# Optimization experiments

Measured on AMD Instinct MI355X. Metric: run time of the kernel, lower is better.

## Reference

```python
import jax, jax.numpy as jnp
import numpy as np

# Hyperparameters matching init_kwargs / repo defaults
MARGIN = 0.2
ALPHA = 0.1          # opt.alpha
OT_ITER = 20         # opt.OT_iteration
BETA = 0.5           # IPOT temperature (hardcoded in repo's OT module)
SIM_TYPE = "MISA"    # opt.sim_type_dot
MAX_VIOLATION = True
EPS = 1e-12

N_IMAGE = 128
N_REG = 36
D = 1024
MAX_WORD = 60


def _matchmap_sim(M):
    # M: (n_image, n_regions, n_word)
    if SIM_TYPE == "SISA":
        return M.mean(axis=2).mean(axis=1)
    elif SIM_TYPE == "MISA":
        return M.max(axis=1).mean(axis=1)
    elif SIM_TYPE == "SIMA":
        return M.max(axis=2).mean(axis=1)
    raise ValueError


def _ipot_distance(C, n, m):
    # C: (bs, n, m) cosine-distance cost; IPOT with uniform marginals.
    bs = C.shape[0]
    # Torch code detaches T, so no gradient flows through the iteration.
    A = jnp.exp(-jax.lax.stop_gradient(C) / BETA)

    def body(_, carry):
        T, sigma = carry
        Q = A * T                                            # (bs, n, m)
        delta = 1.0 / (n * jnp.matmul(Q, sigma))             # (bs, n, 1)
        sigma = 1.0 / (m * jnp.matmul(Q.transpose(0, 2, 1), delta))  # (bs, m, 1)
        T = delta * Q * sigma.transpose(0, 2, 1)
        return (T, sigma)

    T0 = jnp.ones((bs, n, m), C.dtype)
    s0 = jnp.ones((bs, m, 1), C.dtype) / m
    T, _ = jax.lax.fori_loop(0, OT_ITER, body, (T0, s0))
    T = jax.lax.stop_gradient(T)
    # batch_trace(C^T T) == sum(C * T) per batch element
    return -jnp.sum(C * T, axis=(1, 2))                      # (bs,)


def _scores(im, s, cap_lens):
    n_reg = im.shape[1]
    imn = im / (jnp.linalg.norm(im, axis=2, keepdims=True) + EPS)
    lens = np.asarray(cap_lens)
    sims, sims_ot = [], []
    for i in range(s.shape[0]):  # ragged per-caption loop (as in original)
        n_word = int(lens[i])
        cap = s[i, :n_word, :]                               # (w, d)
        # matchmap: bmm(images, cap^T) -> (n_image, n_regions, n_word)
        M = jnp.einsum('brd,wd->brw', im, cap)
        sims.append(_matchmap_sim(M))
        capn = cap / (jnp.linalg.norm(cap, axis=1, keepdims=True) + EPS)
        # cost_matrix_batch_torch(cap^T, img^T).transpose -> (n_image, n_reg, n_word)
        C = 1.0 - jnp.einsum('brd,wd->brw', imn, capn)
        sims_ot.append(_ipot_distance(C, n_reg, n_word))
    return jnp.stack(sims, axis=1), jnp.stack(sims_ot, axis=1)  # (n_img, n_cap)


def _loss(im, s, cap_lens):
    scores, scores_ot = _scores(im, s, cap_lens)
    n = scores.shape[0]
    eye = jnp.eye(n, dtype=bool)

    def costs(sc):
        d = jnp.diag(sc)[:, None]                            # (n, 1)
        cs = jnp.clip(MARGIN + sc - d, 0.0)                  # caption-side
        ci = jnp.clip(MARGIN + sc - d.T, 0.0)                # image-side
        cs = jnp.where(eye, 0.0, cs)
        ci = jnp.where(eye, 0.0, ci)
        return cs, ci

    cost_s, cost_im = costs(scores)
    cost_s_ot, cost_im_ot = costs(scores_ot)
    cost_s = cost_s + ALPHA * cost_s_ot
    cost_im = cost_im + ALPHA * cost_im_ot
    if MAX_VIOLATION:
        cost_s = cost_s.max(axis=1)
        cost_im = cost_im.max(axis=0)
        cost_s_ot = cost_s_ot.max(axis=1)
        cost_im_ot = cost_im_ot.max(axis=0)
    return (cost_s.sum() + cost_im.sum(), cost_s_ot.sum() + cost_im_ot.sum())


def setup_inputs() -> dict:
    key = jax.random.key(0)
    k1, k2, k3 = jax.random.split(key, 3)
    im = jax.random.normal(k1, (N_IMAGE, N_REG, D), dtype=jnp.float32)
    s = jax.random.normal(k2, (N_IMAGE, MAX_WORD, D), dtype=jnp.float32)
    rng = np.random.default_rng(0)
    s_l = np.asarray(rng.integers(10, MAX_WORD + 1, size=N_IMAGE), dtype=np.int64)
    x = jax.random.normal(k3, (1,), dtype=jnp.float32)  # unused by forward math
    return {"im": im, "s": s, "s_l": s_l, "x": x}


def reference(im, s, s_l, x):
    return _loss(im, s, s_l)
```

## Files before the change

kernel.cpp:

```cpp
#include <hip/hip_runtime.h>
#include <hip/hip_bf16.h>
#include <math.h>

#define N_IMAGE 128
#define N_REG   36
#define DIM     1024
#define MAX_WORD 60
#define OT_ITERS 20
#define MARGIN_F 0.2f
#define ALPHA_F  0.1f
#define EPS_F    1e-12f

#define APAN  16384
#define AIMG  (3 * APAN)
#define BCAP  (4 * APAN)

typedef short bf16x8 __attribute__((ext_vector_type(8)));
typedef float f32x4  __attribute__((ext_vector_type(4)));
typedef float f32x2  __attribute__((ext_vector_type(2)));


__device__ __forceinline__ unsigned int pkbf2(float a, float b) {
    union { __hip_bfloat162 h2; unsigned int u; } cv;
    cv.h2 = __float22bfloat162_rn(make_float2(a, b));
    return cv.u;
}
__device__ __forceinline__ float lo16(unsigned int u) { return __int_as_float((int)(u << 16)); }
__device__ __forceinline__ float hi16(unsigned int u) { return __int_as_float((int)(u & 0xFFFF0000u)); }

#define SWZ(x, pat) __int_as_float(__builtin_amdgcn_ds_swizzle(__float_as_int(x), (pat)))
#define BPERM(a, x) __int_as_float(__builtin_amdgcn_ds_bpermute((a), __float_as_int(x)))

__device__ __forceinline__ float bfly16_sum(float x) {
    x += SWZ(x, 0x041F);
    x += SWZ(x, 0x081F);
    x += SWZ(x, 0x101F);
    x += SWZ(x, 0x201F);
    return x;
}

__device__ __forceinline__ float xq_sum(float x) {
    x += SWZ(x, 0x401F);
    const int xaddr = (((int)(threadIdx.x & 63) ^ 32) << 2);
    x += BPERM(xaddr, x);
    return x;
}
__device__ __forceinline__ float xq_max(float x) {
    x = fmaxf(x, SWZ(x, 0x401F));
    const int xaddr = (((int)(threadIdx.x & 63) ^ 32) << 2);
    x = fmaxf(x, BPERM(xaddr, x));
    return x;
}
__device__ __forceinline__ float bfly64_sum(float x) {
    return xq_sum(bfly16_sum(x));
}


__global__ __launch_bounds__(256) void pack_kernel(
    const float* __restrict__ im, const float* __restrict__ s,
    float* __restrict__ inv_im, float* __restrict__ inv_cap,
    float* __restrict__ out,
    unsigned short* __restrict__ imp, unsigned short* __restrict__ sp) {

    const int pid = blockIdx.x;
    const int tid = threadIdx.x;
    if (pid == 0 && tid == 0) { out[0] = 0.0f; out[1] = 0.0f; }

    const int w = tid >> 6, lane = tid & 63, q = lane >> 4, l15 = lane & 15;
    const bool isim = (pid < 384);
    int obj, p, nvalid;
    const float* src;
    unsigned short* dst;
    if (isim) {
        obj = pid / 3; p = pid % 3;
        src = im + (size_t)obj * 36 * DIM;
        dst = imp + (size_t)obj * AIMG + (size_t)p * APAN;
        nvalid = 36;
    } else {
        const int k = pid - 384;
        obj = k >> 2; p = k & 3;
        src = s + (size_t)obj * 60 * DIM;
        dst = sp + (size_t)obj * BCAP + (size_t)p * APAN;
        nvalid = 60;
    }
    const int row = p * 16 + l15;
    const bool valid = (row < nvalid);

    float ss = 0.0f;
    #pragma unroll
    for (int i = 0; i < 4; ++i) {
        const int c = w * 4 + i;
        #pragma unroll
        for (int h = 0; h < 2; ++h) {
            float4 v0 = make_float4(0.f, 0.f, 0.f, 0.f), v1 = v0;
            if (valid) {
                const float* rp = src + (size_t)row * DIM + c * 64 + h * 32 + q * 8;
                v0 = *(const float4*)rp;
                v1 = *(const float4*)(rp + 4);
            }
            ss += v0.x * v0.x + v0.y * v0.y + v0.z * v0.z + v0.w * v0.w
                + v1.x * v1.x + v1.y * v1.y + v1.z * v1.z + v1.w * v1.w;
            uint4 o;
            o.x = pkbf2(v0.x, v0.y); o.y = pkbf2(v0.z, v0.w);
            o.z = pkbf2(v1.x, v1.y); o.w = pkbf2(v1.z, v1.w);
            *(uint4*)(dst + (size_t)c * 1024 + h * 512 + q * 128 + l15 * 8) = o;
        }
    }
    ss = xq_sum(ss);
    __shared__ float sh[4][16];
    if (lane < 16) sh[w][lane] = ss;
    __syncthreads();
    if (tid < 16) {
        const float t = sh[0][tid] + sh[1][tid] + sh[2][tid] + sh[3][tid];
        const int r = p * 16 + tid;
        if (r < nvalid) {
            const float inv = 1.0f / (sqrtf(t) + EPS_F);
            if (isim) inv_im[obj * 36 + r] = inv;
            else      inv_cap[obj * 60 + r] = inv;
        }
    }
}


__global__ void norms_kernel(const float* __restrict__ im, const float* __restrict__ s,
                             float* __restrict__ inv_im, float* __restrict__ inv_cap,
                             float* __restrict__ out) {
    if (blockIdx.x == 0 && threadIdx.x == 0) { out[0] = 0.0f; out[1] = 0.0f; }
    const int NIM = N_IMAGE * N_REG;
    const int NS  = N_IMAGE * MAX_WORD;
    int row  = blockIdx.x * 4 + (threadIdx.x >> 6);
    int lane = threadIdx.x & 63;
    if (row >= NIM + NS) return;
    const bool isim = (row < NIM);
    const float* base = isim ? (im + (size_t)row * DIM)
                             : (s  + (size_t)(row - NIM) * DIM);
    const float4* b4 = (const float4*)base;
    float acc = 0.0f;
    for (int k = lane; k < DIM / 4; k += 64) {
        float4 v = b4[k];
        acc += v.x * v.x + v.y * v.y + v.z * v.z + v.w * v.w;
    }
    for (int off = 32; off; off >>= 1) acc += __shfl_down(acc, off, 64);
    if (lane == 0) {
        float inv = 1.0f / (sqrtf(acc) + EPS_F);
        if (isim) inv_im[row] = inv;
        else      inv_cap[row - NIM] = inv;
    }
}


template <int CT>
__device__ __forceinline__ void build_apk(
    f32x4 (&acc)[3 * CT], const float* invImS, const float* invCapS,
    int m, int wv, int q, int l15,
    unsigned int (*apk)[(CT + 1) / 2], float* mxv, bool* vw) {

    constexpr int PK = (CT + 1) / 2;
    float icap2[CT];
    #pragma unroll
    for (int ct = 0; ct < CT; ++ct) {
        const int w = ct * 16 + l15;
        vw[ct]    = (w < m);
        icap2[ct] = (w < 60) ? 2.0f * invCapS[w] : 0.0f;
    }
    #pragma unroll
    for (int ct = 0; ct < CT; ++ct) mxv[ct] = -3e38f;

    #pragma unroll
    for (int j = 0; j < 12; ++j) {
        const int rt = j >> 2, p = j & 3;
        const int r  = rt * 16 + q * 4 + p;
        const bool rowok = (rt < 2) || (q == 0);
        const float iir = rowok ? invImS[wv * 36 + (r < 36 ? r : 0)] : 0.0f;
        float av[CT];
        #pragma unroll
        for (int ct = 0; ct < CT; ++ct) {
            const float Mv = acc[rt * CT + ct][p];
            mxv[ct] = fmaxf(mxv[ct], rowok ? Mv : -3e38f);
            const bool ok = rowok && vw[ct];
            av[ct] = ok ? __expf(fmaf(Mv, iir * icap2[ct], -2.0f)) : 0.0f;
        }
        #pragma unroll
        for (int pk = 0; pk < PK; ++pk)
            apk[j][pk] = pkbf2(av[2 * pk], (2 * pk + 1 < CT) ? av[2 * pk + 1] : 0.0f);
    }

    {
        const int baddr = l15 << 2;
        #pragma unroll
        for (int pk = 0; pk < PK; ++pk) {
            const int r0 = __builtin_amdgcn_ds_bpermute(baddr, (int)apk[8][pk]);
            const int r1 = __builtin_amdgcn_ds_bpermute(baddr, (int)apk[9][pk]);
            const int r2 = __builtin_amdgcn_ds_bpermute(baddr, (int)apk[10][pk]);
            const int r3 = __builtin_amdgcn_ds_bpermute(baddr, (int)apk[11][pk]);
            const int lo = (q & 1) ? r1 : r0;
            const int hi = (q & 1) ? r3 : r2;
            apk[8][pk] = (unsigned int)((q & 2) ? hi : lo);
        }
    }
}


template <int CT>
__device__ __forceinline__ float ot_iterate(
    f32x2 (*af)[(CT + 1) / 2], const bool* vw, float mf, float inv_m) {

    constexpr int PK = (CT + 1) / 2;
    f32x2 t2[9][PK];
    f32x2 sig2[PK];
    #pragma unroll
    for (int pk = 0; pk < PK; ++pk) {
        const bool v0 = vw[2 * pk];
        const bool v1 = (2 * pk + 1 < CT) && vw[2 * pk + 1];
        sig2[pk].x = v0 ? inv_m : 0.0f;
        sig2[pk].y = v1 ? inv_m : 0.0f;
        #pragma unroll
        for (int j = 0; j < 9; ++j) {
            t2[j][pk].x = v0 ? mf : 0.0f;
            t2[j][pk].y = v1 ? mf : 0.0f;
        }
    }

    for (int it = 0; it < OT_ITERS; ++it) {
        f32x2 s2[PK], csum[PK];
        #pragma unroll
        for (int pk = 0; pk < PK; ++pk) {
            s2[pk]   = sig2[pk] * sig2[pk];
            csum[pk] = (f32x2){0.0f, 0.0f};
        }
        #pragma unroll
        for (int j = 0; j < 9; ++j) {
            f32x2 at[PK];
            #pragma unroll
            for (int pk = 0; pk < PK; ++pk)
                at[pk] = af[j][pk] * t2[j][pk];
            f32x2 u2 = at[0] * s2[0];
            #pragma unroll
            for (int pk = 1; pk < PK; ++pk) u2 += at[pk] * s2[pk];
            const float R  = bfly16_sum(u2.x + u2.y);
            const float dl = __builtin_amdgcn_rcpf(36.0f * R);
            f32x2 dl2; dl2.x = dl; dl2.y = dl;
            #pragma unroll
            for (int pk = 0; pk < PK; ++pk) {
                const f32x2 tn = at[pk] * (dl2 * sig2[pk]);
                t2[j][pk] = tn;
                csum[pk] += tn;
            }
        }
        #pragma unroll
        for (int pk = 0; pk < PK; ++pk) {
            const float cx = xq_sum(csum[pk].x);
            const float cy = xq_sum(csum[pk].y);
            const bool v0 = vw[2 * pk];
            const bool v1 = (2 * pk + 1 < CT) && vw[2 * pk + 1];
            sig2[pk].x = v0 ? __builtin_amdgcn_rcpf(mf * cx) : 0.0f;
            sig2[pk].y = v1 ? __builtin_amdgcn_rcpf(mf * cy) : 0.0f;
        }
    }

    float pp = 0.0f;
    #pragma unroll
    for (int j = 0; j < 9; ++j) {
        #pragma unroll
        for (int pk = 0; pk < PK; ++pk) {
            const float cvx = -0.5f * __logf(fmaxf(af[j][pk].x, 1e-30f));
            pp = fmaf(cvx, t2[j][pk].x * sig2[pk].x, pp);
            if (2 * pk + 1 < CT) {
                const float cvy = -0.5f * __logf(fmaxf(af[j][pk].y, 1e-30f));
                pp = fmaf(cvy, t2[j][pk].y * sig2[pk].y, pp);
            }
        }
    }
    return bfly64_sum(pp);
}


template <int CT>
__device__ __forceinline__ void misa_write(
    const float* mxv, const bool* vw, float inv_m, int lane,
    float* __restrict__ S, int b, int cap) {
    float sp = 0.0f;
    #pragma unroll
    for (int ct = 0; ct < CT; ++ct) {
        float v = xq_max(mxv[ct]);
        sp += vw[ct] ? v : 0.0f;
    }
    sp = bfly64_sum(sp);
    if (lane == 0) S[(size_t)b * N_IMAGE + cap] = sp * inv_m * 0.25f;
}


template <int CT>
__device__ __forceinline__ void gemm_core(
    const unsigned short* __restrict__ imp, const unsigned short* __restrict__ sp,
    int cap, int b0, int wv, int q, int l15, f32x4 (&acc)[3 * CT]) {

    const unsigned short* Ab = imp + (size_t)(b0 + wv) * AIMG + (q * 128 + l15 * 8);
    const unsigned short* Bb = sp  + (size_t)cap * BCAP        + (q * 128 + l15 * 8);

    #pragma unroll
    for (int t = 0; t < 3 * CT; ++t) acc[t] = (f32x4){0.f, 0.f, 0.f, 0.f};

    bf16x8 a0[3], bf0[CT], a1[3], bf1[CT];
    #pragma unroll
    for (int rt = 0; rt < 3; ++rt) a0[rt] = *(const bf16x8*)(Ab + rt * APAN);
    #pragma unroll
    for (int ct = 0; ct < CT; ++ct) bf0[ct] = *(const bf16x8*)(Bb + ct * APAN);

    #pragma unroll 1
    for (int c = 0; c < 16; ++c) {
        const unsigned short* Ac = Ab + c * 1024;
        const unsigned short* Bc = Bb + c * 1024;
        #pragma unroll
        for (int rt = 0; rt < 3; ++rt) a1[rt] = *(const bf16x8*)(Ac + rt * APAN + 512);
        #pragma unroll
        for (int ct = 0; ct < CT; ++ct) bf1[ct] = *(const bf16x8*)(Bc + ct * APAN + 512);
        #pragma unroll
        for (int rt = 0; rt < 3; ++rt)
            #pragma unroll
            for (int ct = 0; ct < CT; ++ct)
                acc[rt * CT + ct] = __builtin_amdgcn_mfma_f32_16x16x32_bf16(
                    a0[rt], bf0[ct], acc[rt * CT + ct], 0, 0, 0);
        const int cn = (c < 15) ? c + 1 : 15;
        const unsigned short* An = Ab + cn * 1024;
        const unsigned short* Bn = Bb + cn * 1024;
        #pragma unroll
        for (int rt = 0; rt < 3; ++rt) a0[rt] = *(const bf16x8*)(An + rt * APAN);
        #pragma unroll
        for (int ct = 0; ct < CT; ++ct) bf0[ct] = *(const bf16x8*)(Bn + ct * APAN);
        #pragma unroll
        for (int rt = 0; rt < 3; ++rt)
            #pragma unroll
            for (int ct = 0; ct < CT; ++ct)
                acc[rt * CT + ct] = __builtin_amdgcn_mfma_f32_16x16x32_bf16(
                    a1[rt], bf1[ct], acc[rt * CT + ct], 0, 0, 0);
    }
}


template <int CT>
__device__ __forceinline__ void pair_body_fast(
    const unsigned short* __restrict__ imp, const unsigned short* __restrict__ sp,
    const float* invImS, const float* invCapS,
    int cap, int b0, int m,
    float* __restrict__ S, float* __restrict__ SOT) {

    const int tid  = threadIdx.x;
    const int lane = tid & 63;
    const int wv   = tid >> 6;
    const int q    = lane >> 4;
    const int l15  = lane & 15;
    const float mf    = (float)m;
    const float inv_m = 1.0f / mf;
    constexpr int PK = (CT + 1) / 2;

    f32x4 acc[3 * CT];
    gemm_core<CT>(imp, sp, cap, b0, wv, q, l15, acc);

    __syncthreads();

    unsigned int apk[12][PK];
    float mxv[CT]; bool vw[CT];
    build_apk<CT>(acc, invImS, invCapS, m, wv, q, l15, apk, mxv, vw);

    f32x2 af[9][PK];
    #pragma unroll
    for (int j = 0; j < 9; ++j)
        #pragma unroll
        for (int pk = 0; pk < PK; ++pk) {
            af[j][pk].x = lo16(apk[j][pk]);
            af[j][pk].y = hi16(apk[j][pk]);
        }

    const int b = b0 + wv;
    misa_write<CT>(mxv, vw, inv_m, lane, S, b, cap);
    const float pp = ot_iterate<CT>(af, vw, mf, inv_m);
    if (lane == 0) SOT[(size_t)b * N_IMAGE + cap] = -pp;
}

__global__ __launch_bounds__(256, 4)
void pair_fast(const unsigned short* __restrict__ imp,
               const unsigned short* __restrict__ sp,
               const int* __restrict__ s_l,
               const float* __restrict__ inv_im, const float* __restrict__ inv_cap,
               float* __restrict__ S, float* __restrict__ SOT) {
    const int cap = blockIdx.x;
    const int b0  = blockIdx.y * 4;
    const int tid = threadIdx.x;

    __shared__ float invImS[144];
    __shared__ float invCapS[60];
    if (tid < 144) invImS[tid] = inv_im[b0 * 36 + tid];
    else if (tid < 204) invCapS[tid - 144] = inv_cap[cap * 60 + (tid - 144)];

    const int m  = s_l[cap];
    const int CT = __builtin_amdgcn_readfirstlane((m + 15) >> 4);
    switch (CT) {
    case 1: pair_body_fast<1>(imp, sp, invImS, invCapS, cap, b0, m, S, SOT); break;
    case 2: pair_body_fast<2>(imp, sp, invImS, invCapS, cap, b0, m, S, SOT); break;
    case 3: pair_body_fast<3>(imp, sp, invImS, invCapS, cap, b0, m, S, SOT); break;
    default: pair_body_fast<4>(imp, sp, invImS, invCapS, cap, b0, m, S, SOT); break;
    }
}


template <int CT>
__device__ __forceinline__ void pair_body_slow(
    const float* __restrict__ im, const float* __restrict__ s,
    char* smem, const float* invImS, const float* invCapS,
    int cap, int b0, int m,
    float* __restrict__ S, float* __restrict__ SOT) {

    const int tid  = threadIdx.x;
    const int lane = tid & 63;
    const int wv   = tid >> 6;
    const int q    = lane >> 4;
    const int l15  = lane & 15;
    const int q4   = tid & 15;
    const int row0 = tid >> 4;
    const float mf    = (float)m;
    const float inv_m = 1.0f / mf;
    constexpr int PK = (CT + 1) / 2;

    const char* sA = smem;
    const char* sB = smem + 27648;

    f32x4 acc[3 * CT];
    #pragma unroll
    for (int t = 0; t < 3 * CT; ++t) acc[t] = (f32x4){0.f, 0.f, 0.f, 0.f};

    for (int c = 0; c < 16; ++c) {
        const int col = c * 64 + q4 * 4;
        #pragma unroll
        for (int img = 0; img < 4; ++img) {
            #pragma unroll
            for (int j = 0; j < 3; ++j) {
                const int r = row0 + 16 * j;
                if (j < 2 || row0 < 4) {
                    const size_t ro = (size_t)(b0 * 36 + img * 36 + r) * 1024 + col;
                    float4 v = *(const float4*)(im + ro);
                    uint2 w2; w2.x = pkbf2(v.x, v.y); w2.y = pkbf2(v.z, v.w);
                    *(uint2*)(smem + (img * 48 + r) * 144 + q4 * 8) = w2;
                }
            }
        }
        #pragma unroll
        for (int j = 0; j < CT; ++j) {
            const int r = row0 + 16 * j;
            if (CT < 4 || j < 3 || row0 < 12) {
                const size_t ro = (size_t)(cap * 60 + r) * 1024 + col;
                float4 v = *(const float4*)(s + ro);
                uint2 w2; w2.x = pkbf2(v.x, v.y); w2.y = pkbf2(v.z, v.w);
                *(uint2*)(smem + (192 + r) * 144 + q4 * 8) = w2;
            }
        }
        __syncthreads();
        #pragma unroll
        for (int h = 0; h < 2; ++h) {
            bf16x8 bfr[CT];
            #pragma unroll
            for (int ct = 0; ct < CT; ++ct)
                bfr[ct] = *(const bf16x8*)(sB + (ct * 16 + l15) * 144 + h * 64 + q * 16);
            #pragma unroll
            for (int rt = 0; rt < 3; ++rt) {
                bf16x8 afr = *(const bf16x8*)(sA + (wv * 48 + rt * 16 + l15) * 144 + h * 64 + q * 16);
                #pragma unroll
                for (int ct = 0; ct < CT; ++ct)
                    acc[rt * CT + ct] = __builtin_amdgcn_mfma_f32_16x16x32_bf16(
                        afr, bfr[ct], acc[rt * CT + ct], 0, 0, 0);
            }
        }
        __syncthreads();
    }

    unsigned int apk[12][PK];
    float mxv[CT]; bool vw[CT];
    build_apk<CT>(acc, invImS, invCapS, m, wv, q, l15, apk, mxv, vw);

    f32x2 af[9][PK];
    #pragma unroll
    for (int j = 0; j < 9; ++j)
        #pragma unroll
        for (int pk = 0; pk < PK; ++pk) {
            af[j][pk].x = lo16(apk[j][pk]);
            af[j][pk].y = hi16(apk[j][pk]);
        }

    const int b = b0 + wv;
    misa_write<CT>(mxv, vw, inv_m, lane, S, b, cap);
    const float pp = ot_iterate<CT>(af, vw, mf, inv_m);
    if (lane == 0) SOT[(size_t)b * N_IMAGE + cap] = -pp;
}

__global__ __launch_bounds__(256, 4)
void pair_slow(const float* __restrict__ im, const float* __restrict__ s,
               const int* __restrict__ s_l,
               const float* __restrict__ inv_im, const float* __restrict__ inv_cap,
               float* __restrict__ S, float* __restrict__ SOT) {
    const int cap = blockIdx.x;
    const int b0  = blockIdx.y * 4;
    const int tid = threadIdx.x;

    __shared__ __align__(16) char smem[36864];
    __shared__ float invImS[144];
    __shared__ float invCapS[60];

    if (tid < 144) invImS[tid] = inv_im[b0 * 36 + tid];
    else if (tid < 204) invCapS[tid - 144] = inv_cap[cap * 60 + (tid - 144)];

    const int m = s_l[cap];
    {
        float4 z = make_float4(0.f, 0.f, 0.f, 0.f);
        #pragma unroll
        for (int j = 0; j < 9; ++j)
            *(float4*)(smem + (tid + j * 256) * 16) = z;
    }
    __syncthreads();

    const int CT = __builtin_amdgcn_readfirstlane((m + 15) >> 4);
    switch (CT) {
    case 1: pair_body_slow<1>(im, s, smem, invImS, invCapS, cap, b0, m, S, SOT); break;
    case 2: pair_body_slow<2>(im, s, smem, invImS, invCapS, cap, b0, m, S, SOT); break;
    case 3: pair_body_slow<3>(im, s, smem, invImS, invCapS, cap, b0, m, S, SOT); break;
    default: pair_body_slow<4>(im, s, smem, invImS, invCapS, cap, b0, m, S, SOT); break;
    }
}


__global__ void loss_kernel(const float* __restrict__ S, const float* __restrict__ SOT,
                            float* __restrict__ out) {
    const int j = blockIdx.x;
    const int t = threadIdx.x;
    __shared__ float sh[4][2];
    const float db  = S[j * 129];
    const float dob = SOT[j * 129];
    float rv = 0.f, rov = 0.f, cv = 0.f, cov = 0.f;
    if (t != j) {
        float cs  = fmaxf(0.0f, MARGIN_F + S[j * 128 + t] - db);
        float cso = fmaxf(0.0f, MARGIN_F + SOT[j * 128 + t] - dob);
        rv = cs + ALPHA_F * cso;  rov = cso;
        float ci  = fmaxf(0.0f, MARGIN_F + S[t * 128 + j] - db);
        float cio = fmaxf(0.0f, MARGIN_F + SOT[t * 128 + j] - dob);
        cv = ci + ALPHA_F * cio;  cov = cio;
    }
    for (int off = 32; off; off >>= 1) {
        rv  = fmaxf(rv,  __shfl_down(rv,  off, 64));
        rov = fmaxf(rov, __shfl_down(rov, off, 64));
        cv  = fmaxf(cv,  __shfl_down(cv,  off, 64));
        cov = fmaxf(cov, __shfl_down(cov, off, 64));
    }
    if ((t & 63) == 0) {
        sh[0][t >> 6] = rv; sh[1][t >> 6] = rov;
        sh[2][t >> 6] = cv; sh[3][t >> 6] = cov;
    }
    __syncthreads();
    if (t == 0) {
        float a0 = fmaxf(sh[0][0], sh[0][1]) + fmaxf(sh[2][0], sh[2][1]);
        float a1 = fmaxf(sh[1][0], sh[1][1]) + fmaxf(sh[3][0], sh[3][1]);
        atomicAdd(&out[0], a0);
        atomicAdd(&out[1], a1);
    }
}

extern "C" void kernel_launch(void* const* d_in, const int* in_sizes, int n_in,
                              void* d_out, int out_size, void* d_ws, size_t ws_size,
                              hipStream_t stream) {
    const float* im  = (const float*)d_in[0];
    const float* s   = (const float*)d_in[1];
    const int*   s_l = (const int*)d_in[2];
    float* out = (float*)d_out;
    float* ws  = (float*)d_ws;

    float* inv_im  = ws;
    float* inv_cap = ws + 4608;
    float* S       = ws + 12288;
    float* SOT     = ws + 28672;
    unsigned short* imp = (unsigned short*)((char*)d_ws + 180224);
    unsigned short* sp  = imp + (size_t)N_IMAGE * AIMG;
    const size_t need_fast = 180224 +
        ((size_t)N_IMAGE * AIMG + (size_t)N_IMAGE * BCAP) * 2;

    if (ws_size >= need_fast) {
        pack_kernel<<<dim3(896), dim3(256), 0, stream>>>(
            im, s, inv_im, inv_cap, out, imp, sp);
        pair_fast<<<dim3(N_IMAGE, N_IMAGE / 4), dim3(256), 0, stream>>>(
            imp, sp, s_l, inv_im, inv_cap, S, SOT);
    } else {
        norms_kernel<<<dim3((4608 + 7680) / 4), dim3(256), 0, stream>>>(
            im, s, inv_im, inv_cap, out);
        pair_slow<<<dim3(N_IMAGE, N_IMAGE / 4), dim3(256), 0, stream>>>(
            im, s, s_l, inv_im, inv_cap, S, SOT);
    }
    loss_kernel<<<dim3(N_IMAGE), dim3(128), 0, stream>>>(S, SOT, out);
}
```

Baseline: 308.0 us.

## Cut register pressure to raise occupancy and use DPP for 16-lane reductions

The OT kernel now keeps the exp-cost matrix packed as bf16 pairs and unpacks it on the fly each iteration, instead of holding an unpacked float copy in registers. The GEMM core drops its software double-buffered prefetch in favour of plain per-half loads. Launch bounds are raised from 4 to 5 blocks per SM. The 16-lane butterfly sum switches from ds_swizzle to DPP row operations. Together these aim to lower VGPR use so more waves fit per CU and to shorten the latency of the reductions. The cost is extra unpack ALU work inside the iteration loop and less hiding of load latency in the GEMM.

```diff
diff --git a/kernel.cpp b/kernel.cpp
--- a/kernel.cpp
+++ b/kernel.cpp
@@ -30,12 +30,14 @@
 
 #define SWZ(x, pat) __int_as_float(__builtin_amdgcn_ds_swizzle(__float_as_int(x), (pat)))
 #define BPERM(a, x) __int_as_float(__builtin_amdgcn_ds_bpermute((a), __float_as_int(x)))
+#define DPPADD(x, ctrl) \
+    ((x) + __int_as_float(__builtin_amdgcn_update_dpp(0, __float_as_int(x), (ctrl), 0xf, 0xf, true)))
 
 __device__ __forceinline__ float bfly16_sum(float x) {
-    x += SWZ(x, 0x041F);
-    x += SWZ(x, 0x081F);
-    x += SWZ(x, 0x101F);
-    x += SWZ(x, 0x201F);
+    x = DPPADD(x, 0xB1);
+    x = DPPADD(x, 0x4E);
+    x = DPPADD(x, 0x124);
+    x = DPPADD(x, 0x128);
     return x;
 }
 
@@ -203,7 +205,7 @@
 
 template <int CT>
 __device__ __forceinline__ float ot_iterate(
-    f32x2 (*af)[(CT + 1) / 2], const bool* vw, float mf, float inv_m) {
+    const unsigned int (*apk)[(CT + 1) / 2], const bool* vw, float mf, float inv_m) {
 
     constexpr int PK = (CT + 1) / 2;
     f32x2 t2[9][PK];
@@ -232,8 +234,12 @@
         for (int j = 0; j < 9; ++j) {
             f32x2 at[PK];
             #pragma unroll
-            for (int pk = 0; pk < PK; ++pk)
-                at[pk] = af[j][pk] * t2[j][pk];
+            for (int pk = 0; pk < PK; ++pk) {
+                f32x2 a2;
+                a2.x = lo16(apk[j][pk]);
+                a2.y = hi16(apk[j][pk]);
+                at[pk] = a2 * t2[j][pk];
+            }
             f32x2 u2 = at[0] * s2[0];
             #pragma unroll
             for (int pk = 1; pk < PK; ++pk) u2 += at[pk] * s2[pk];
@@ -263,10 +269,12 @@
     for (int j = 0; j < 9; ++j) {
         #pragma unroll
         for (int pk = 0; pk < PK; ++pk) {
-            const float cvx = -0.5f * __logf(fmaxf(af[j][pk].x, 1e-30f));
+            const float ax = lo16(apk[j][pk]);
+            const float cvx = -0.5f * __logf(fmaxf(ax, 1e-30f));
             pp = fmaf(cvx, t2[j][pk].x * sig2[pk].x, pp);
             if (2 * pk + 1 < CT) {
-                const float cvy = -0.5f * __logf(fmaxf(af[j][pk].y, 1e-30f));
+                const float ay = hi16(apk[j][pk]);
+                const float cvy = -0.5f * __logf(fmaxf(ay, 1e-30f));
                 pp = fmaf(cvy, t2[j][pk].y * sig2[pk].y, pp);
             }
         }
@@ -301,39 +309,24 @@
     #pragma unroll
     for (int t = 0; t < 3 * CT; ++t) acc[t] = (f32x4){0.f, 0.f, 0.f, 0.f};
 
-    bf16x8 a0[3], bf0[CT], a1[3], bf1[CT];
-    #pragma unroll
-    for (int rt = 0; rt < 3; ++rt) a0[rt] = *(const bf16x8*)(Ab + rt * APAN);
-    #pragma unroll
-    for (int ct = 0; ct < CT; ++ct) bf0[ct] = *(const bf16x8*)(Bb + ct * APAN);
-
     #pragma unroll 1
     for (int c = 0; c < 16; ++c) {
-        const unsigned short* Ac = Ab + c * 1024;
-        const unsigned short* Bc = Bb + c * 1024;
-        #pragma unroll
-        for (int rt = 0; rt < 3; ++rt) a1[rt] = *(const bf16x8*)(Ac + rt * APAN + 512);
-        #pragma unroll
-        for (int ct = 0; ct < CT; ++ct) bf1[ct] = *(const bf16x8*)(Bc + ct * APAN + 512);
-        #pragma unroll
-        for (int rt = 0; rt < 3; ++rt)
-            #pragma unroll
-            for (int ct = 0; ct < CT; ++ct)
-                acc[rt * CT + ct] = __builtin_amdgcn_mfma_f32_16x16x32_bf16(
-                    a0[rt], bf0[ct], acc[rt * CT + ct], 0, 0, 0);
-        const int cn = (c < 15) ? c + 1 : 15;
-        const unsigned short* An = Ab + cn * 1024;
-        const unsigned short* Bn = Bb + cn * 1024;
-        #pragma unroll
-        for (int rt = 0; rt < 3; ++rt) a0[rt] = *(const bf16x8*)(An + rt * APAN);
-        #pragma unroll
-        for (int ct = 0; ct < CT; ++ct) bf0[ct] = *(const bf16x8*)(Bn + ct * APAN);
-        #pragma unroll
-        for (int rt = 0; rt < 3; ++rt)
-            #pragma unroll
-            for (int ct = 0; ct < CT; ++ct)
-                acc[rt * CT + ct] = __builtin_amdgcn_mfma_f32_16x16x32_bf16(
-                    a1[rt], bf1[ct], acc[rt * CT + ct], 0, 0, 0);
+        #pragma unroll
+        for (int h = 0; h < 2; ++h) {
+            const unsigned short* Ac = Ab + c * 1024 + h * 512;
+            const unsigned short* Bc = Bb + c * 1024 + h * 512;
+            bf16x8 a0[3], bf0[CT];
+            #pragma unroll
+            for (int rt = 0; rt < 3; ++rt) a0[rt] = *(const bf16x8*)(Ac + rt * APAN);
+            #pragma unroll
+            for (int ct = 0; ct < CT; ++ct) bf0[ct] = *(const bf16x8*)(Bc + ct * APAN);
+            #pragma unroll
+            for (int rt = 0; rt < 3; ++rt)
+                #pragma unroll
+                for (int ct = 0; ct < CT; ++ct)
+                    acc[rt * CT + ct] = __builtin_amdgcn_mfma_f32_16x16x32_bf16(
+                        a0[rt], bf0[ct], acc[rt * CT + ct], 0, 0, 0);
+        }
     }
 }
 
@@ -363,22 +356,13 @@
     float mxv[CT]; bool vw[CT];
     build_apk<CT>(acc, invImS, invCapS, m, wv, q, l15, apk, mxv, vw);
 
-    f32x2 af[9][PK];
-    #pragma unroll
-    for (int j = 0; j < 9; ++j)
-        #pragma unroll
-        for (int pk = 0; pk < PK; ++pk) {
-            af[j][pk].x = lo16(apk[j][pk]);
-            af[j][pk].y = hi16(apk[j][pk]);
-        }
-
     const int b = b0 + wv;
     misa_write<CT>(mxv, vw, inv_m, lane, S, b, cap);
-    const float pp = ot_iterate<CT>(af, vw, mf, inv_m);
+    const float pp = ot_iterate<CT>(apk, vw, mf, inv_m);
     if (lane == 0) SOT[(size_t)b * N_IMAGE + cap] = -pp;
 }
 
-__global__ __launch_bounds__(256, 4)
+__global__ __launch_bounds__(256, 5)
 void pair_fast(const unsigned short* __restrict__ imp,
                const unsigned short* __restrict__ sp,
                const int* __restrict__ s_l,
@@ -477,18 +461,9 @@
     float mxv[CT]; bool vw[CT];
     build_apk<CT>(acc, invImS, invCapS, m, wv, q, l15, apk, mxv, vw);
 
-    f32x2 af[9][PK];
-    #pragma unroll
-    for (int j = 0; j < 9; ++j)
-        #pragma unroll
-        for (int pk = 0; pk < PK; ++pk) {
-            af[j][pk].x = lo16(apk[j][pk]);
-            af[j][pk].y = hi16(apk[j][pk]);
-        }
-
     const int b = b0 + wv;
     misa_write<CT>(mxv, vw, inv_m, lane, S, b, cap);
-    const float pp = ot_iterate<CT>(af, vw, mf, inv_m);
+    const float pp = ot_iterate<CT>(apk, vw, mf, inv_m);
     if (lane == 0) SOT[(size_t)b * N_IMAGE + cap] = -pp;
 }
 
```

Result: faster. 289.5 us (-6.0%).

## Schedule pair blocks longest-caption-first and use DPP for 16-lane reductions

Applied to the files above, without the earlier changes.

Adds a tiny sort kernel that ranks captions by length, descending, and remaps pair_fast to a 1D grid so the longest captions' blocks are dispatched first. This is meant to reduce tail imbalance from ragged caption lengths (CT 1..4 tiles). It also replaces the ds_swizzle butterfly in bfly16_sum with DPP row ops, which avoids LDS-crossbar latency. The cost is an extra kernel launch and an extra indirection through perm.

```diff
diff --git a/kernel.cpp b/kernel.cpp
--- a/kernel.cpp
+++ b/kernel.cpp
@@ -30,12 +30,14 @@
 
 #define SWZ(x, pat) __int_as_float(__builtin_amdgcn_ds_swizzle(__float_as_int(x), (pat)))
 #define BPERM(a, x) __int_as_float(__builtin_amdgcn_ds_bpermute((a), __float_as_int(x)))
+#define DPPADD(x, ctrl) \
+    ((x) + __int_as_float(__builtin_amdgcn_update_dpp(0, __float_as_int(x), (ctrl), 0xf, 0xf, true)))
 
 __device__ __forceinline__ float bfly16_sum(float x) {
-    x += SWZ(x, 0x041F);
-    x += SWZ(x, 0x081F);
-    x += SWZ(x, 0x101F);
-    x += SWZ(x, 0x201F);
+    x = DPPADD(x, 0xB1);
+    x = DPPADD(x, 0x4E);
+    x = DPPADD(x, 0x124);
+    x = DPPADD(x, 0x128);
     return x;
 }
 
@@ -53,6 +55,18 @@
 }
 __device__ __forceinline__ float bfly64_sum(float x) {
     return xq_sum(bfly16_sum(x));
+}
+
+
+__global__ void sort_kernel(const int* __restrict__ s_l, int* __restrict__ perm) {
+    const int t = threadIdx.x;
+    const int mt = s_l[t];
+    int rank = 0;
+    for (int j = 0; j < N_IMAGE; ++j) {
+        const int mj = s_l[j];
+        rank += (mj > mt) || (mj == mt && j < t);
+    }
+    perm[rank] = t;
 }
 
 
@@ -382,10 +396,12 @@
 void pair_fast(const unsigned short* __restrict__ imp,
                const unsigned short* __restrict__ sp,
                const int* __restrict__ s_l,
+               const int* __restrict__ perm,
                const float* __restrict__ inv_im, const float* __restrict__ inv_cap,
                float* __restrict__ S, float* __restrict__ SOT) {
-    const int cap = blockIdx.x;
-    const int b0  = blockIdx.y * 4;
+    const int bid = blockIdx.x;
+    const int cap = perm[bid >> 5];
+    const int b0  = (bid & 31) * 4;
     const int tid = threadIdx.x;
 
     __shared__ float invImS[144];
@@ -575,16 +591,18 @@
     float* inv_cap = ws + 4608;
     float* S       = ws + 12288;
     float* SOT     = ws + 28672;
-    unsigned short* imp = (unsigned short*)((char*)d_ws + 180224);
+    int*   perm    = (int*)(ws + 45056);
+    unsigned short* imp = (unsigned short*)((char*)d_ws + 180736);
     unsigned short* sp  = imp + (size_t)N_IMAGE * AIMG;
-    const size_t need_fast = 180224 +
+    const size_t need_fast = 180736 +
         ((size_t)N_IMAGE * AIMG + (size_t)N_IMAGE * BCAP) * 2;
 
     if (ws_size >= need_fast) {
+        sort_kernel<<<dim3(1), dim3(128), 0, stream>>>(s_l, perm);
         pack_kernel<<<dim3(896), dim3(256), 0, stream>>>(
             im, s, inv_im, inv_cap, out, imp, sp);
-        pair_fast<<<dim3(N_IMAGE, N_IMAGE / 4), dim3(256), 0, stream>>>(
-            imp, sp, s_l, inv_im, inv_cap, S, SOT);
+        pair_fast<<<dim3(N_IMAGE * N_IMAGE / 4), dim3(256), 0, stream>>>(
+            imp, sp, s_l, perm, inv_im, inv_cap, S, SOT);
     } else {
         norms_kernel<<<dim3((4608 + 7680) / 4), dim3(256), 0, stream>>>(
             im, s, inv_im, inv_cap, out);
```

Result: faster. 263.6 us (-14.4%).
